# Performance work log

Measured on AMD Instinct MI355X. Metric: run time of the kernel, lower is better.

## Reference

```python
import jax, jax.numpy as jnp
import numpy as np

D_MODEL = 512
NUM_HEADS = 8
D_HEAD = D_MODEL // NUM_HEADS
SCALE = 1.0 / np.sqrt(D_HEAD)


def setup_inputs() -> dict:
    key = jax.random.key(0)
    ks = jax.random.split(key, 16)
    B, T, D = 8, 1024, D_MODEL
    std = 1.0 / np.sqrt(D)
    inp = {
        'x': jax.random.normal(ks[0], (B, T, D), jnp.float32),
        'pos_enc': jax.random.normal(ks[1], (1, 2 * T - 1, D), jnp.float32),
        'Wq': jax.random.normal(ks[2], (D, D), jnp.float32) * std,
        'bq': jnp.zeros((D,), jnp.float32),
        'Wk': jax.random.normal(ks[3], (D, D), jnp.float32) * std,
        'bk': jnp.zeros((D,), jnp.float32),
        'Wv': jax.random.normal(ks[4], (D, D), jnp.float32) * std,
        'bv': jnp.zeros((D,), jnp.float32),
        'Wpos': jax.random.normal(ks[5], (D, D), jnp.float32) * std,
        'pos_bias_u': jax.random.normal(ks[6], (NUM_HEADS, D_HEAD), jnp.float32) * std,
        'pos_bias_v': jax.random.normal(ks[7], (NUM_HEADS, D_HEAD), jnp.float32) * std,
        'Wo': jax.random.normal(ks[8], (D, D), jnp.float32) * std,
        'bo': jnp.zeros((D,), jnp.float32),
    }
    return inp


def _relative_shift(x):
    # x: (batch, heads, time, 2*time-1) -> (batch, heads, time, time)
    b, h, t, _ = x.shape
    x = jnp.pad(x, ((0, 0), (0, 0), (0, 0), (1, 0)))  # (b,h,t,2t)
    x = x.reshape(b, h, 2 * t, t)
    x = x[:, :, 1:, :]
    x = x.reshape(b, h, t, 2 * t - 1)
    return x[:, :, :, :t]


def reference(x, pos_enc, Wq, bq, Wk, bk, Wv, bv, Wpos, pos_bias_u, pos_bias_v, Wo, bo):
    B, T, D = x.shape
    H, Dh = NUM_HEADS, D_HEAD
    q = (x @ Wq + bq).reshape(B, T, H, Dh).transpose(0, 2, 1, 3)  # (B,H,T,Dh)
    k = (x @ Wk + bk).reshape(B, T, H, Dh).transpose(0, 2, 1, 3)
    v = (x @ Wv + bv).reshape(B, T, H, Dh).transpose(0, 2, 1, 3)
    p = (pos_enc @ Wpos).reshape(1, -1, H, Dh).transpose(0, 2, 1, 3)  # (1,H,2T-1,Dh)

    q_u = q + pos_bias_u[None, :, None, :]
    q_v = q + pos_bias_v[None, :, None, :]

    content_score = jnp.einsum('bhtd,bhsd->bhts', q_u, k)         # (B,H,T,T)
    pos_score = jnp.einsum('bhtd,xhpd->bhtp', q_v, p)             # (B,H,T,2T-1)
    pos_score = _relative_shift(pos_score)                         # (B,H,T,T)

    scores = (content_score + pos_score) * SCALE
    attn = jax.nn.softmax(scores, axis=-1)
    out = jnp.einsum('bhts,bhsd->bhtd', attn, v)                   # (B,H,T,Dh)
    out = out.transpose(0, 2, 1, 3).reshape(B, T, D)
    return out @ Wo + bo
```

## Files before the change

### kernel.cpp

```cpp
#include <hip/hip_runtime.h>
#include <hip/hip_bf16.h>

#define T_SEQ 1024
#define D_MODEL 512
#define N_HEADS 8
#define D_HEAD 64
#define KSCALE 0.1803368801111244f

typedef unsigned short ushort_t;
typedef short s16x8 __attribute__((ext_vector_type(8)));
typedef float f32x4 __attribute__((ext_vector_type(4)));

__device__ inline f32x4 mfma16(s16x8 a, s16x8 b, f32x4 c) {
    return __builtin_amdgcn_mfma_f32_16x16x32_bf16(a, b, c, 0, 0, 0);
}

__device__ inline ushort_t f2bf(float f) {
    union { float f; unsigned u; } v; v.f = f;
    unsigned r = v.u + 0x7FFFu + ((v.u >> 16) & 1u);
    return (ushort_t)(r >> 16);
}
__device__ inline void cvt4(const float4 f, ushort_t* t) {
    t[0] = f2bf(f.x); t[1] = f2bf(f.y); t[2] = f2bf(f.z); t[3] = f2bf(f.w);
}
__device__ inline s16x8 pack8(const ushort_t* t) {
    s16x8 r;
    #pragma unroll
    for (int e = 0; e < 8; ++e) r[e] = (short)t[e];
    return r;
}

__device__ inline void gl_lds16(const ushort_t* g, ushort_t* l) {
    __builtin_amdgcn_global_load_lds(
        (const __attribute__((address_space(1))) unsigned*)g,
        (__attribute__((address_space(3))) unsigned*)l, 16, 0, 0);
}

__global__ __launch_bounds__(256) void prep(
    const float* __restrict__ x, const float* __restrict__ pos,
    const float* __restrict__ W0, const float* __restrict__ W1,
    const float* __restrict__ W2, const float* __restrict__ W3,
    const float* __restrict__ W4,
    ushort_t* __restrict__ xb, ushort_t* __restrict__ posb,
    ushort_t* __restrict__ WT)
{
    __shared__ float T[64][68];
    const int bx = blockIdx.x;
    const int tid = threadIdx.x;
    if (bx < 2560) {
        const size_t N1 = (size_t)8192 * 512;
        size_t e = ((size_t)bx * 256 + tid) * 8;
        ushort_t tmp[8];
        if (e < N1) {
            const float4* s = (const float4*)(x + e);
            cvt4(s[0], tmp); cvt4(s[1], tmp + 4);
            *(s16x8*)(xb + e) = pack8(tmp);
        } else {
            size_t e2 = e - N1;
            int row = (int)(e2 >> 9);
            if (row < 2047) {
                const float4* s = (const float4*)(pos + e2);
                cvt4(s[0], tmp); cvt4(s[1], tmp + 4);
            } else {
                #pragma unroll
                for (int i = 0; i < 8; ++i) tmp[i] = 0;
            }
            *(s16x8*)(posb + e2) = pack8(tmp);
        }
    } else {
        const int bz = bx - 2560;
        const int z = bz >> 6;
        const int rem = bz & 63;
        const int n0 = (rem & 7) * 64, k0 = (rem >> 3) * 64;
        const float* W = (z == 0) ? W0 : (z == 1) ? W1
                       : (z == 2) ? W2 : (z == 3) ? W3 : W4;
        const int rr = tid >> 2, cc = (tid & 3) * 16;

        const float* src = W + (size_t)(k0 + rr) * 512 + n0 + cc;
        *(float4*)&T[rr][cc + 0]  = *(const float4*)(src);
        *(float4*)&T[rr][cc + 4]  = *(const float4*)(src + 4);
        *(float4*)&T[rr][cc + 8]  = *(const float4*)(src + 8);
        *(float4*)&T[rr][cc + 12] = *(const float4*)(src + 12);
        __syncthreads();

        ushort_t tmp[16];
        #pragma unroll
        for (int e = 0; e < 16; ++e) tmp[e] = f2bf(T[cc + e][rr]);
        ushort_t* dst = WT + ((size_t)z * 512 + n0 + rr) * 512 + k0 + cc;
        *(s16x8*)dst       = pack8(tmp);
        *(s16x8*)(dst + 8) = pack8(tmp + 8);
    }
}

__global__ __launch_bounds__(256) void gemm_qkvp(
    const ushort_t* __restrict__ xb, const ushort_t* __restrict__ posb,
    const ushort_t* __restrict__ WT,
    const float* __restrict__ bq, const float* __restrict__ bk,
    const float* __restrict__ bv,
    const float* __restrict__ pbu, const float* __restrict__ pbv,
    ushort_t* __restrict__ Qu, ushort_t* __restrict__ Qv,
    ushort_t* __restrict__ Ko, ushort_t* __restrict__ VoT,
    ushort_t* __restrict__ Po)
{
    const int tid = threadIdx.x;
    const bool is_p = (blockIdx.x == 12);
    int row0, col0;
    const ushort_t* A;
    const ushort_t* B;
    if (is_p) {
        row0 = ((int)blockIdx.y >> 2) * 128;
        col0 = ((int)blockIdx.y & 3) * 128;
        A = posb;
        B = WT + (size_t)3 * 512 * 512;
    } else {
        row0 = blockIdx.y * 128;
        col0 = blockIdx.x * 128;
        A = xb;
        B = WT;
    }
    const int w = tid >> 6, lane = tid & 63;
    const int quad = lane >> 4, lanelo = lane & 15;
    const int wr = w >> 1, wc = w & 1;

    __shared__ ushort_t AsF[128 * 64];
    __shared__ ushort_t BsF[128 * 64];

    f32x4 acc[4][4] = {};

    for (int k0 = 0; k0 < 512; k0 += 64) {
        __syncthreads();
        #pragma unroll
        for (int i = 0; i < 4; ++i) {
            const int L = i * 256 + tid;
            const int r = L >> 3, j = (L & 7) * 8;
            ushort_t* lbase = AsF + (size_t)(i * 256 + (tid & ~63)) * 8;
            gl_lds16(A + (size_t)(row0 + r) * 512 + k0 + j, lbase);
            ushort_t* lbase2 = BsF + (size_t)(i * 256 + (tid & ~63)) * 8;
            gl_lds16(B + (size_t)(col0 + r) * 512 + k0 + j, lbase2);
        }
        __syncthreads();

        #pragma unroll
        for (int ks = 0; ks < 2; ++ks) {
            s16x8 af[4], bf[4];
            #pragma unroll
            for (int i = 0; i < 4; ++i)
                af[i] = *(const s16x8*)(AsF + (size_t)(64 * wr + 16 * i + lanelo) * 64 + ks * 32 + quad * 8);
            #pragma unroll
            for (int j = 0; j < 4; ++j)
                bf[j] = *(const s16x8*)(BsF + (size_t)(64 * wc + 16 * j + lanelo) * 64 + ks * 32 + quad * 8);
            #pragma unroll
            for (int i = 0; i < 4; ++i)
                #pragma unroll
                for (int j = 0; j < 4; ++j)
                    acc[i][j] = mfma16(af[i], bf[j], acc[i][j]);
        }
    }

    if (is_p) {
        #pragma unroll
        for (int j = 0; j < 4; ++j) {
            int c = col0 + 64 * wc + 16 * j + lanelo;
            #pragma unroll
            for (int i = 0; i < 4; ++i)
                #pragma unroll
                for (int r = 0; r < 4; ++r) {
                    int row = row0 + 64 * wr + 16 * i + 4 * quad + r;
                    Po[(size_t)row * 512 + c] = f2bf(acc[i][j][r]);
                }
        }
        return;
    }

    const int set = col0 >> 9;
    const int cbase = (col0 & 511) + 64 * wc;
    if (set == 0) {
        #pragma unroll
        for (int j = 0; j < 4; ++j) {
            int c = cbase + 16 * j + lanelo;
            float vbq = bq[c], vu = pbu[c], vv = pbv[c];
            #pragma unroll
            for (int i = 0; i < 4; ++i)
                #pragma unroll
                for (int r = 0; r < 4; ++r) {
                    int row = row0 + 64 * wr + 16 * i + 4 * quad + r;
                    size_t o = (size_t)row * 512 + c;
                    float aq = acc[i][j][r] + vbq;
                    Qu[o] = f2bf((aq + vu) * KSCALE);
                    Qv[o] = f2bf((aq + vv) * KSCALE);
                }
        }
    } else if (set == 1) {
        #pragma unroll
        for (int j = 0; j < 4; ++j) {
            int c = cbase + 16 * j + lanelo;
            float vbk = bk[c];
            #pragma unroll
            for (int i = 0; i < 4; ++i)
                #pragma unroll
                for (int r = 0; r < 4; ++r) {
                    int row = row0 + 64 * wr + 16 * i + 4 * quad + r;
                    Ko[(size_t)row * 512 + c] = f2bf(acc[i][j][r] + vbk);
                }
        }
    } else {
        const int b_idx = row0 >> 10;
        #pragma unroll
        for (int j = 0; j < 4; ++j) {
            int c = cbase + 16 * j + lanelo;
            int hh = c >> 6, d = c & 63;
            float vbb = bv[c];
            #pragma unroll
            for (int i = 0; i < 4; ++i) {
                int t = (row0 & 1023) + 64 * wr + 16 * i + 4 * quad;
                ushort4 vp;
                vp.x = f2bf(acc[i][j][0] + vbb);
                vp.y = f2bf(acc[i][j][1] + vbb);
                vp.z = f2bf(acc[i][j][2] + vbb);
                vp.w = f2bf(acc[i][j][3] + vbb);
                *(ushort4*)(VoT + ((size_t)((b_idx * 8 + hh) * 64 + d)) * 1024 + t) = vp;
            }
        }
    }
}

__global__ __launch_bounds__(256) void attn_mfma(
    const ushort_t* __restrict__ Qu, const ushort_t* __restrict__ Qv,
    const ushort_t* __restrict__ Kb, const ushort_t* __restrict__ VT,
    const ushort_t* __restrict__ Pb,
    ushort_t* __restrict__ AOb)
{
    const int tid = threadIdx.x;
    const int t0 = blockIdx.x * 64;
    const int h  = blockIdx.y;
    const int b  = blockIdx.z;
    const int w = tid >> 6, lane = tid & 63;
    const int quad = lane >> 4, lanelo = lane & 15;
    const int sr = tid >> 2, sc = (tid & 3) * 16;

    __shared__ ushort_t Kt[64][72];
    __shared__ ushort_t VtT[64][72];
    __shared__ ushort_t Pt[128][72];
    __shared__ ushort_t Ps[64][72];

    const size_t qrow = (size_t)(b * T_SEQ + t0 + 16 * w + lanelo) * 512 + h * 64;
    s16x8 qu[2], qv[2];
    qu[0] = *(const s16x8*)(Qu + qrow + quad * 8);
    qu[1] = *(const s16x8*)(Qu + qrow + 32 + quad * 8);
    qv[0] = *(const s16x8*)(Qv + qrow + quad * 8);
    qv[1] = *(const s16x8*)(Qv + qrow + 32 + quad * 8);

    f32x4 acc_o[4] = {};
    float l_part[4] = {0.f, 0.f, 0.f, 0.f};

    const int u_base = lanelo + 63 - 4 * quad;
    const ushort_t* VTbh = VT + ((size_t)((b * 8 + h) * 64)) * 1024;
    const ushort_t* Kbh  = Kb + (size_t)b * T_SEQ * 512 + (size_t)h * 64;
    const int pr_base = 960 - t0;

    {
        const ushort_t* kp = Kbh + (size_t)sr * 512 + sc;
        *(s16x8*)&Kt[sr][sc]     = *(const s16x8*)kp;
        *(s16x8*)&Kt[sr][sc + 8] = *(const s16x8*)(kp + 8);
        const ushort_t* vp = VTbh + (size_t)sr * 1024 + sc;
        *(s16x8*)&VtT[sr][sc]     = *(const s16x8*)vp;
        *(s16x8*)&VtT[sr][sc + 8] = *(const s16x8*)(vp + 8);
        const int pr_r = tid >> 1, pr_c = (tid & 1) * 32;
        const int slot = (pr_base + pr_r) & 127;
        const ushort_t* gp = Pb + (size_t)(pr_base + pr_r) * 512 + h * 64 + pr_c;
        *(s16x8*)&Pt[slot][pr_c +  0] = *(const s16x8*)(gp +  0);
        *(s16x8*)&Pt[slot][pr_c +  8] = *(const s16x8*)(gp +  8);
        *(s16x8*)&Pt[slot][pr_c + 16] = *(const s16x8*)(gp + 16);
        *(s16x8*)&Pt[slot][pr_c + 24] = *(const s16x8*)(gp + 24);
    }

    for (int it = 0; it < 16; ++it) {
        const int s0 = it * 64;
        __syncthreads();

        s16x8 kp0, kp1, vp0, vp1, pp0, pp1;
        const bool more = (it < 15);
        if (more) {
            const ushort_t* kp = Kbh + (size_t)(s0 + 64 + sr) * 512 + sc;
            kp0 = *(const s16x8*)kp;
            kp1 = *(const s16x8*)(kp + 8);
            const ushort_t* vp = VTbh + (size_t)sr * 1024 + s0 + 64 + sc;
            vp0 = *(const s16x8*)vp;
            vp1 = *(const s16x8*)(vp + 8);
            const ushort_t* gp = Pb + (size_t)(pr_base + s0 + 128 + sr) * 512 + h * 64 + sc;
            pp0 = *(const s16x8*)gp;
            pp1 = *(const s16x8*)(gp + 8);
        }

        const int pbase = (pr_base + s0) & 127;
        f32x4 acc_c[4] = {};
        f32x4 acc_g[5] = {};
        #pragma unroll
        for (int ks = 0; ks < 2; ++ks) {
            #pragma unroll
            for (int tn = 0; tn < 4; ++tn) {
                s16x8 kf = *(const s16x8*)&Kt[tn * 16 + lanelo][ks * 32 + quad * 8];
                acc_c[tn] = mfma16(qu[ks], kf, acc_c[tn]);
            }
            #pragma unroll
            for (int i = 0; i < 5; ++i) {
                int prow = (pbase + (3 - w + i) * 16 + lanelo) & 127;
                s16x8 pf = *(const s16x8*)&Pt[prow][ks * 32 + quad * 8];
                acc_g[i] = mfma16(qv[ks], pf, acc_g[i]);
            }
        }

        float p[4][4];
        #pragma unroll
        for (int r = 0; r < 4; ++r) {
            int u = u_base - r;
            int srcl = (quad << 4) | (u & 15);
            bool hi = (u >= 64);
            #pragma unroll
            for (int tn = 0; tn < 4; ++tn) {
                float v0 = __shfl(acc_g[tn][r], srcl);
                float v1 = __shfl(acc_g[tn + 1][r], srcl);
                float e = __builtin_amdgcn_exp2f(acc_c[tn][r] + (hi ? v1 : v0));
                p[tn][r] = e;
                l_part[r] += e;
            }
        }
        #pragma unroll
        for (int tn = 0; tn < 4; ++tn)
            #pragma unroll
            for (int r = 0; r < 4; ++r)
                Ps[16 * w + 4 * quad + r][tn * 16 + lanelo] = f2bf(p[tn][r]);
        asm volatile("s_waitcnt lgkmcnt(0)" ::: "memory");

        #pragma unroll
        for (int ks = 0; ks < 2; ++ks) {
            s16x8 af = *(const s16x8*)&Ps[16 * w + lanelo][ks * 32 + quad * 8];
            #pragma unroll
            for (int dt = 0; dt < 4; ++dt) {
                s16x8 vb = *(const s16x8*)&VtT[dt * 16 + lanelo][ks * 32 + quad * 8];
                acc_o[dt] = mfma16(af, vb, acc_o[dt]);
            }
        }

        __syncthreads();
        if (more) {
            *(s16x8*)&Kt[sr][sc]      = kp0;
            *(s16x8*)&Kt[sr][sc + 8]  = kp1;
            *(s16x8*)&VtT[sr][sc]     = vp0;
            *(s16x8*)&VtT[sr][sc + 8] = vp1;
            const int slot = (pr_base + s0 + 128 + sr) & 127;
            *(s16x8*)&Pt[slot][sc]     = pp0;
            *(s16x8*)&Pt[slot][sc + 8] = pp1;
        }
    }

    float inv[4];
    #pragma unroll
    for (int r = 0; r < 4; ++r) {
        float l = l_part[r];
        l += __shfl_xor(l, 1);
        l += __shfl_xor(l, 2);
        l += __shfl_xor(l, 4);
        l += __shfl_xor(l, 8);
        inv[r] = 1.0f / l;
    }

    __syncthreads();
    #pragma unroll
    for (int r = 0; r < 4; ++r)
        #pragma unroll
        for (int dt = 0; dt < 4; ++dt)
            Ps[16 * w + 4 * quad + r][dt * 16 + lanelo] = f2bf(acc_o[dt][r] * inv[r]);
    __syncthreads();
    {
        ushort_t* dst = AOb + (size_t)(b * T_SEQ + t0 + sr) * 512 + h * 64 + sc;
        *(s16x8*)dst       = *(const s16x8*)&Ps[sr][sc];
        *(s16x8*)(dst + 8) = *(const s16x8*)&Ps[sr][sc + 8];
    }
}

__global__ __launch_bounds__(256) void gemm_out(
    const ushort_t* __restrict__ A, const ushort_t* __restrict__ WTo,
    const float* __restrict__ bias, float* __restrict__ C)
{
    const int tid = threadIdx.x;
    const int col0 = blockIdx.x * 128;
    const int row0 = blockIdx.y * 128;
    const int w = tid >> 6, lane = tid & 63;
    const int quad = lane >> 4, lanelo = lane & 15;
    const int wr = w >> 1, wc = w & 1;

    __shared__ ushort_t AsF[128 * 64];
    __shared__ ushort_t BsF[128 * 64];

    f32x4 acc[4][4] = {};

    for (int k0 = 0; k0 < 512; k0 += 64) {
        __syncthreads();
        #pragma unroll
        for (int i = 0; i < 4; ++i) {
            const int L = i * 256 + tid;
            const int r = L >> 3, j = (L & 7) * 8;
            ushort_t* lbase = AsF + (size_t)(i * 256 + (tid & ~63)) * 8;
            gl_lds16(A + (size_t)(row0 + r) * 512 + k0 + j, lbase);
            ushort_t* lbase2 = BsF + (size_t)(i * 256 + (tid & ~63)) * 8;
            gl_lds16(WTo + (size_t)(col0 + r) * 512 + k0 + j, lbase2);
        }
        __syncthreads();

        #pragma unroll
        for (int ks = 0; ks < 2; ++ks) {
            s16x8 af[4], bf[4];
            #pragma unroll
            for (int i = 0; i < 4; ++i)
                af[i] = *(const s16x8*)(AsF + (size_t)(64 * wr + 16 * i + lanelo) * 64 + ks * 32 + quad * 8);
            #pragma unroll
            for (int j = 0; j < 4; ++j)
                bf[j] = *(const s16x8*)(BsF + (size_t)(64 * wc + 16 * j + lanelo) * 64 + ks * 32 + quad * 8);
            #pragma unroll
            for (int i = 0; i < 4; ++i)
                #pragma unroll
                for (int j = 0; j < 4; ++j)
                    acc[i][j] = mfma16(af[i], bf[j], acc[i][j]);
        }
    }

    #pragma unroll
    for (int j = 0; j < 4; ++j) {
        int c = col0 + 64 * wc + 16 * j + lanelo;
        float vb = bias[c];
        #pragma unroll
        for (int i = 0; i < 4; ++i)
            #pragma unroll
            for (int r = 0; r < 4; ++r) {
                int row = row0 + 64 * wr + 16 * i + 4 * quad + r;
                C[(size_t)row * 512 + c] = acc[i][j][r] + vb;
            }
    }
}

extern "C" void kernel_launch(void* const* d_in, const int* in_sizes, int n_in,
                              void* d_out, int out_size, void* d_ws, size_t ws_size,
                              hipStream_t stream) {
    const float* x       = (const float*)d_in[0];
    const float* pos_enc = (const float*)d_in[1];
    const float* Wq      = (const float*)d_in[2];
    const float* bq      = (const float*)d_in[3];
    const float* Wk      = (const float*)d_in[4];
    const float* bk      = (const float*)d_in[5];
    const float* Wv      = (const float*)d_in[6];
    const float* bv      = (const float*)d_in[7];
    const float* Wpos    = (const float*)d_in[8];
    const float* pbu     = (const float*)d_in[9];
    const float* pbv     = (const float*)d_in[10];
    const float* Wo      = (const float*)d_in[11];
    const float* bo      = (const float*)d_in[12];
    float* out = (float*)d_out;

    const size_t M  = 8 * T_SEQ;
    const size_t SZ = M * D_MODEL;

    char* ws = (char*)d_ws;
    ushort_t* xb   = (ushort_t*)ws;              ws += SZ * 2;
    ushort_t* posb = (ushort_t*)ws;              ws += (size_t)2048 * 512 * 2;
    ushort_t* Qu_b = (ushort_t*)ws;              ws += SZ * 2;
    ushort_t* Qv_b = (ushort_t*)ws;              ws += SZ * 2;
    ushort_t* K_b  = (ushort_t*)ws;              ws += SZ * 2;
    ushort_t* VT_b = (ushort_t*)ws;              ws += SZ * 2;
    ushort_t* P_b  = (ushort_t*)ws;              ws += (size_t)2048 * 512 * 2;
    ushort_t* WT   = (ushort_t*)ws;              ws += (size_t)5 * 512 * 512 * 2;
    ushort_t* AOb  = (ushort_t*)ws;              ws += SZ * 2;

    dim3 blk(256);

    hipLaunchKernelGGL(prep, dim3(2880), blk, 0, stream,
                       x, pos_enc, Wq, Wk, Wv, Wpos, Wo, xb, posb, WT);

    hipLaunchKernelGGL(gemm_qkvp, dim3(13, 64), blk, 0, stream,
                       xb, posb, WT, bq, bk, bv, pbu, pbv,
                       Qu_b, Qv_b, K_b, VT_b, P_b);

    hipLaunchKernelGGL(attn_mfma, dim3(16, 8, 8), blk, 0, stream,
                       Qu_b, Qv_b, K_b, VT_b, P_b, AOb);

    hipLaunchKernelGGL(gemm_out, dim3(4, 64), blk, 0, stream,
                       AOb, WT + (size_t)4 * 512 * 512, bo, out);
}
```

Measured before the change: 230.7 us.

## Derive Qv in attention from Qu and swizzle attention LDS tiles

The projection kernel now writes only Qu. The attention kernel rebuilds Qv in registers by adding the scaled difference of the two position biases, which removes one full bf16 Q-sized write and read through global memory. All attention shared-memory tiles (K, V^T, P ring, probability tile) switch from padded 72-wide rows to unpadded 64-wide rows with an XOR swizzle of the 16-byte chunks, meant to avoid LDS bank conflicts while using less shared memory. Qv now picks up an extra bf16 rounding step, since it is computed from the already-rounded Qu.

```diff
diff --git a/kernel.cpp b/kernel.cpp
--- a/kernel.cpp
+++ b/kernel.cpp
@@ -20,6 +20,9 @@
     unsigned r = v.u + 0x7FFFu + ((v.u >> 16) & 1u);
     return (ushort_t)(r >> 16);
 }
+__device__ inline float bf2f(short s) {
+    union { unsigned u; float f; } t; t.u = ((unsigned)(unsigned short)s) << 16; return t.f;
+}
 __device__ inline void cvt4(const float4 f, ushort_t* t) {
     t[0] = f2bf(f.x); t[1] = f2bf(f.y); t[2] = f2bf(f.z); t[3] = f2bf(f.w);
 }
@@ -28,6 +31,10 @@
     #pragma unroll
     for (int e = 0; e < 8; ++e) r[e] = (short)t[e];
     return r;
+}
+
+__device__ inline int lidx(int row, int chunk) {
+    return row * 64 + ((chunk ^ (row & 7)) << 3);
 }
 
 __device__ inline void gl_lds16(const ushort_t* g, ushort_t* l) {
@@ -96,11 +103,9 @@
     const ushort_t* __restrict__ xb, const ushort_t* __restrict__ posb,
     const ushort_t* __restrict__ WT,
     const float* __restrict__ bq, const float* __restrict__ bk,
-    const float* __restrict__ bv,
-    const float* __restrict__ pbu, const float* __restrict__ pbv,
-    ushort_t* __restrict__ Qu, ushort_t* __restrict__ Qv,
-    ushort_t* __restrict__ Ko, ushort_t* __restrict__ VoT,
-    ushort_t* __restrict__ Po)
+    const float* __restrict__ bv, const float* __restrict__ pbu,
+    ushort_t* __restrict__ Qu, ushort_t* __restrict__ Ko,
+    ushort_t* __restrict__ VoT, ushort_t* __restrict__ Po)
 {
     const int tid = threadIdx.x;
     const bool is_p = (blockIdx.x == 12);
@@ -178,16 +183,13 @@
         #pragma unroll
         for (int j = 0; j < 4; ++j) {
             int c = cbase + 16 * j + lanelo;
-            float vbq = bq[c], vu = pbu[c], vv = pbv[c];
+            float vq = bq[c] + pbu[c];
             #pragma unroll
             for (int i = 0; i < 4; ++i)
                 #pragma unroll
                 for (int r = 0; r < 4; ++r) {
                     int row = row0 + 64 * wr + 16 * i + 4 * quad + r;
-                    size_t o = (size_t)row * 512 + c;
-                    float aq = acc[i][j][r] + vbq;
-                    Qu[o] = f2bf((aq + vu) * KSCALE);
-                    Qv[o] = f2bf((aq + vv) * KSCALE);
+                    Qu[(size_t)row * 512 + c] = f2bf((acc[i][j][r] + vq) * KSCALE);
                 }
         }
     } else if (set == 1) {
@@ -225,9 +227,10 @@
 }
 
 __global__ __launch_bounds__(256) void attn_mfma(
-    const ushort_t* __restrict__ Qu, const ushort_t* __restrict__ Qv,
+    const ushort_t* __restrict__ Qu,
     const ushort_t* __restrict__ Kb, const ushort_t* __restrict__ VT,
     const ushort_t* __restrict__ Pb,
+    const float* __restrict__ pbu, const float* __restrict__ pbv,
     ushort_t* __restrict__ AOb)
 {
     const int tid = threadIdx.x;
@@ -236,19 +239,27 @@
     const int b  = blockIdx.z;
     const int w = tid >> 6, lane = tid & 63;
     const int quad = lane >> 4, lanelo = lane & 15;
-    const int sr = tid >> 2, sc = (tid & 3) * 16;
-
-    __shared__ ushort_t Kt[64][72];
-    __shared__ ushort_t VtT[64][72];
-    __shared__ ushort_t Pt[128][72];
-    __shared__ ushort_t Ps[64][72];
+    const int sr = tid >> 2;
+    const int scch = (tid & 3) * 2;
+    const int sc = scch * 8;
+
+    __shared__ ushort_t Kt[64 * 64];
+    __shared__ ushort_t VtT[64 * 64];
+    __shared__ ushort_t Pt[128 * 64];
+    __shared__ ushort_t Ps[64 * 64];
 
     const size_t qrow = (size_t)(b * T_SEQ + t0 + 16 * w + lanelo) * 512 + h * 64;
     s16x8 qu[2], qv[2];
     qu[0] = *(const s16x8*)(Qu + qrow + quad * 8);
     qu[1] = *(const s16x8*)(Qu + qrow + 32 + quad * 8);
-    qv[0] = *(const s16x8*)(Qv + qrow + quad * 8);
-    qv[1] = *(const s16x8*)(Qv + qrow + 32 + quad * 8);
+    #pragma unroll
+    for (int e = 0; e < 8; ++e) {
+        int k0i = h * 64 + quad * 8 + e;
+        float d0 = (pbv[k0i] - pbu[k0i]) * KSCALE;
+        float d1 = (pbv[k0i + 32] - pbu[k0i + 32]) * KSCALE;
+        qv[0][e] = (short)f2bf(bf2f(qu[0][e]) + d0);
+        qv[1][e] = (short)f2bf(bf2f(qu[1][e]) + d1);
+    }
 
     f32x4 acc_o[4] = {};
     float l_part[4] = {0.f, 0.f, 0.f, 0.f};
@@ -260,18 +271,18 @@
 
     {
         const ushort_t* kp = Kbh + (size_t)sr * 512 + sc;
-        *(s16x8*)&Kt[sr][sc]     = *(const s16x8*)kp;
-        *(s16x8*)&Kt[sr][sc + 8] = *(const s16x8*)(kp + 8);
+        *(s16x8*)(Kt + lidx(sr, scch))     = *(const s16x8*)kp;
+        *(s16x8*)(Kt + lidx(sr, scch + 1)) = *(const s16x8*)(kp + 8);
         const ushort_t* vp = VTbh + (size_t)sr * 1024 + sc;
-        *(s16x8*)&VtT[sr][sc]     = *(const s16x8*)vp;
-        *(s16x8*)&VtT[sr][sc + 8] = *(const s16x8*)(vp + 8);
-        const int pr_r = tid >> 1, pr_c = (tid & 1) * 32;
+        *(s16x8*)(VtT + lidx(sr, scch))     = *(const s16x8*)vp;
+        *(s16x8*)(VtT + lidx(sr, scch + 1)) = *(const s16x8*)(vp + 8);
+        const int pr_r = tid >> 1, pc0 = (tid & 1) * 4;
         const int slot = (pr_base + pr_r) & 127;
-        const ushort_t* gp = Pb + (size_t)(pr_base + pr_r) * 512 + h * 64 + pr_c;
-        *(s16x8*)&Pt[slot][pr_c +  0] = *(const s16x8*)(gp +  0);
-        *(s16x8*)&Pt[slot][pr_c +  8] = *(const s16x8*)(gp +  8);
-        *(s16x8*)&Pt[slot][pr_c + 16] = *(const s16x8*)(gp + 16);
-        *(s16x8*)&Pt[slot][pr_c + 24] = *(const s16x8*)(gp + 24);
+        const ushort_t* gp = Pb + (size_t)(pr_base + pr_r) * 512 + h * 64 + pc0 * 8;
+        *(s16x8*)(Pt + lidx(slot, pc0))     = *(const s16x8*)(gp +  0);
+        *(s16x8*)(Pt + lidx(slot, pc0 + 1)) = *(const s16x8*)(gp +  8);
+        *(s16x8*)(Pt + lidx(slot, pc0 + 2)) = *(const s16x8*)(gp + 16);
+        *(s16x8*)(Pt + lidx(slot, pc0 + 3)) = *(const s16x8*)(gp + 24);
     }
 
     for (int it = 0; it < 16; ++it) {
@@ -299,13 +310,13 @@
         for (int ks = 0; ks < 2; ++ks) {
             #pragma unroll
             for (int tn = 0; tn < 4; ++tn) {
-                s16x8 kf = *(const s16x8*)&Kt[tn * 16 + lanelo][ks * 32 + quad * 8];
+                s16x8 kf = *(const s16x8*)(Kt + lidx(tn * 16 + lanelo, 4 * ks + quad));
                 acc_c[tn] = mfma16(qu[ks], kf, acc_c[tn]);
             }
             #pragma unroll
             for (int i = 0; i < 5; ++i) {
                 int prow = (pbase + (3 - w + i) * 16 + lanelo) & 127;
-                s16x8 pf = *(const s16x8*)&Pt[prow][ks * 32 + quad * 8];
+                s16x8 pf = *(const s16x8*)(Pt + lidx(prow, 4 * ks + quad));
                 acc_g[i] = mfma16(qv[ks], pf, acc_g[i]);
             }
         }
@@ -328,29 +339,32 @@
         #pragma unroll
         for (int tn = 0; tn < 4; ++tn)
             #pragma unroll
-            for (int r = 0; r < 4; ++r)
-                Ps[16 * w + 4 * quad + r][tn * 16 + lanelo] = f2bf(p[tn][r]);
+            for (int r = 0; r < 4; ++r) {
+                int pr = 16 * w + 4 * quad + r;
+                int ch = 2 * tn + (lanelo >> 3);
+                Ps[pr * 64 + ((ch ^ (pr & 7)) << 3) + (lanelo & 7)] = f2bf(p[tn][r]);
+            }
         asm volatile("s_waitcnt lgkmcnt(0)" ::: "memory");
 
         #pragma unroll
         for (int ks = 0; ks < 2; ++ks) {
-            s16x8 af = *(const s16x8*)&Ps[16 * w + lanelo][ks * 32 + quad * 8];
+            s16x8 af = *(const s16x8*)(Ps + lidx(16 * w + lanelo, 4 * ks + quad));
             #pragma unroll
             for (int dt = 0; dt < 4; ++dt) {
-                s16x8 vb = *(const s16x8*)&VtT[dt * 16 + lanelo][ks * 32 + quad * 8];
+                s16x8 vb = *(const s16x8*)(VtT + lidx(dt * 16 + lanelo, 4 * ks + quad));
                 acc_o[dt] = mfma16(af, vb, acc_o[dt]);
             }
         }
 
         __syncthreads();
         if (more) {
-            *(s16x8*)&Kt[sr][sc]      = kp0;
-            *(s16x8*)&Kt[sr][sc + 8]  = kp1;
-            *(s16x8*)&VtT[sr][sc]     = vp0;
-            *(s16x8*)&VtT[sr][sc + 8] = vp1;
+            *(s16x8*)(Kt + lidx(sr, scch))      = kp0;
+            *(s16x8*)(Kt + lidx(sr, scch + 1))  = kp1;
+            *(s16x8*)(VtT + lidx(sr, scch))     = vp0;
+            *(s16x8*)(VtT + lidx(sr, scch + 1)) = vp1;
             const int slot = (pr_base + s0 + 128 + sr) & 127;
-            *(s16x8*)&Pt[slot][sc]     = pp0;
-            *(s16x8*)&Pt[slot][sc + 8] = pp1;
+            *(s16x8*)(Pt + lidx(slot, scch))     = pp0;
+            *(s16x8*)(Pt + lidx(slot, scch + 1)) = pp1;
         }
     }
 
@@ -369,13 +383,16 @@
     #pragma unroll
     for (int r = 0; r < 4; ++r)
         #pragma unroll
-        for (int dt = 0; dt < 4; ++dt)
-            Ps[16 * w + 4 * quad + r][dt * 16 + lanelo] = f2bf(acc_o[dt][r] * inv[r]);
+        for (int dt = 0; dt < 4; ++dt) {
+            int pr = 16 * w + 4 * quad + r;
+            int ch = 2 * dt + (lanelo >> 3);
+            Ps[pr * 64 + ((ch ^ (pr & 7)) << 3) + (lanelo & 7)] = f2bf(acc_o[dt][r] * inv[r]);
+        }
     __syncthreads();
     {
         ushort_t* dst = AOb + (size_t)(b * T_SEQ + t0 + sr) * 512 + h * 64 + sc;
-        *(s16x8*)dst       = *(const s16x8*)&Ps[sr][sc];
-        *(s16x8*)(dst + 8) = *(const s16x8*)&Ps[sr][sc + 8];
+        *(s16x8*)dst       = *(const s16x8*)(Ps + lidx(sr, scch));
+        *(s16x8*)(dst + 8) = *(const s16x8*)(Ps + lidx(sr, scch + 1));
     }
 }
 
@@ -464,7 +481,6 @@
     ushort_t* xb   = (ushort_t*)ws;              ws += SZ * 2;
     ushort_t* posb = (ushort_t*)ws;              ws += (size_t)2048 * 512 * 2;
     ushort_t* Qu_b = (ushort_t*)ws;              ws += SZ * 2;
-    ushort_t* Qv_b = (ushort_t*)ws;              ws += SZ * 2;
     ushort_t* K_b  = (ushort_t*)ws;              ws += SZ * 2;
     ushort_t* VT_b = (ushort_t*)ws;              ws += SZ * 2;
     ushort_t* P_b  = (ushort_t*)ws;              ws += (size_t)2048 * 512 * 2;
@@ -477,11 +493,11 @@
                        x, pos_enc, Wq, Wk, Wv, Wpos, Wo, xb, posb, WT);
 
     hipLaunchKernelGGL(gemm_qkvp, dim3(13, 64), blk, 0, stream,
-                       xb, posb, WT, bq, bk, bv, pbu, pbv,
-                       Qu_b, Qv_b, K_b, VT_b, P_b);
+                       xb, posb, WT, bq, bk, bv, pbu,
+                       Qu_b, K_b, VT_b, P_b);
 
     hipLaunchKernelGGL(attn_mfma, dim3(16, 8, 8), blk, 0, stream,
-                       Qu_b, Qv_b, K_b, VT_b, P_b, AOb);
+                       Qu_b, K_b, VT_b, P_b, pbu, pbv, AOb);
 
     hipLaunchKernelGGL(gemm_out, dim3(4, 64), blk, 0, stream,
                        AOb, WT + (size_t)4 * 512 * 512, bo, out);
```

New measurement: 205.4 us. 11.0% less time.
